# Kernel optimization log

Measured on AMD Instinct MI355X. Metric: run time of the kernel, lower is better.

## Reference

```python
import jax, jax.numpy as jnp
import numpy as np

B, N, K = 16, 2048, 16          # clouds, points per cloud, knn k
C_IN, C_OUT = 64, 64

def setup_inputs() -> dict:
    key = jax.random.key(0)
    ks = jax.random.split(key, 8)
    s_in = 1.0 / np.sqrt(C_IN)
    return {
        "x": jax.random.normal(ks[0], (B * N, C_IN), jnp.float32),
        "pos": jax.random.normal(ks[1], (B * N, 3), jnp.float32),
        "batch": jnp.repeat(jnp.arange(B, dtype=jnp.int32), N),
        "W_pos": jax.random.normal(ks[2], (3, C_OUT), jnp.float32) / np.sqrt(3.0),
        "b_pos": jnp.zeros((C_OUT,), jnp.float32),
        "W_attn": jax.random.normal(ks[3], (C_OUT, C_OUT), jnp.float32) / np.sqrt(C_OUT),
        "b_attn": jnp.zeros((C_OUT,), jnp.float32),
        "W_val": jax.random.normal(ks[4], (C_IN, C_OUT), jnp.float32) * s_in,
        "W_src": jax.random.normal(ks[5], (C_IN, C_OUT), jnp.float32) * s_in,
        "W_dst": jax.random.normal(ks[6], (C_IN, C_OUT), jnp.float32) * s_in,
    }

def _gather(a, idx):
    # a: [B, N, D], idx: [B, N, K+1] -> [B, N, K+1, D]
    return jax.vmap(lambda ab, ib: ab[ib])(a, idx)

def reference(x, pos, batch, W_pos, b_pos, W_attn, b_attn, W_val, W_src, W_dst):
    # batch is assumed contiguous with equal-size clouds (B clouds of N points),
    # so batch-restricted knn_graph == per-cloud knn after reshape.
    posr = pos.reshape(B, N, 3)
    xr = x.reshape(B, N, C_IN)
    # knn_graph(loop=False): exclude self, then PointTransformerConv re-adds self loops
    d2 = jnp.sum((posr[:, :, None, :] - posr[:, None, :, :]) ** 2, axis=-1)  # [B,N,N]
    d2 = d2 + jnp.eye(N, dtype=d2.dtype) * 1e10
    _, nbr = jax.lax.top_k(-d2, K)                                # [B,N,K] sources j per target i
    self_idx = jnp.broadcast_to(jnp.arange(N)[None, :, None], (B, N, 1))
    nbr = jnp.concatenate([nbr, self_idx], axis=2)                # self loop -> [B,N,K+1]
    alpha_i = xr @ W_dst                                          # lin_dst(x_i)  [B,N,C_OUT]
    alpha_j = _gather(xr @ W_src, nbr)                            # lin_src(x_j)  [B,N,K+1,C_OUT]
    val_j = _gather(xr @ W_val, nbr)                              # lin(x_j)
    pos_j = _gather(posr, nbr)                                    # [B,N,K+1,3]
    delta = (posr[:, :, None, :] - pos_j) @ W_pos + b_pos         # pos_nn(pos_i - pos_j)
    alpha = alpha_i[:, :, None, :] - alpha_j + delta              # subtraction attention
    alpha = alpha @ W_attn + b_attn                               # attn_nn
    alpha = jax.nn.softmax(alpha, axis=2)                         # segment softmax per target i
    out = jnp.sum(alpha * (val_j + delta), axis=2)                # weighted scatter-sum
    return out.reshape(B * N, C_OUT)
```

## Files before the change

kernel.cpp:

```cpp
#include <hip/hip_runtime.h>
#include <math.h>

#define BBATCH 16
#define NPC    2048
#define KNBR   16
#define NPTS   (BBATCH*NPC)
#define NGEMM  512
#define NKNN   512
#define BUFCAP 512

__global__ __launch_bounds__(1024) void prep_kernel(
    const float* __restrict__ Wpos, const float* __restrict__ bpos,
    const float* __restrict__ Wattn, const float* __restrict__ battn,
    const float* __restrict__ Wsrc, const float* __restrict__ Wdst,
    float* __restrict__ Hd, float* __restrict__ Hs,
    float* __restrict__ WP2, float* __restrict__ bb) {
  __shared__ float sW[4096];
  __shared__ float sD[4096];
  __shared__ float sS[4096];
  int t = threadIdx.x;
  ((float4*)sW)[t] = ((const float4*)Wattn)[t];
  ((float4*)sD)[t] = ((const float4*)Wdst)[t];
  ((float4*)sS)[t] = ((const float4*)Wsrc)[t];
  __syncthreads();
  int c = t & 63, r0 = t >> 6;
#pragma unroll
  for (int q = 0; q < 4; ++q) {
    int r = r0 + 16 * q;
    float ad = 0.f, as = 0.f;
    for (int d = 0; d < 64; ++d) {
      float w = sW[d * 64 + c];
      ad += sD[r * 64 + d] * w;
      as += sS[r * 64 + d] * w;
    }
    Hd[r * 64 + c] = ad;
    Hs[r * 64 + c] = as;
  }
  if (t < 64) {
    for (int rr = 0; rr < 3; ++rr) {
      float a = 0.f;
      for (int d = 0; d < 64; ++d) a += Wpos[rr * 64 + d] * sW[d * 64 + t];
      WP2[rr * 64 + t] = a;
    }
    float a = battn[t];
    for (int d = 0; d < 64; ++d) a += bpos[d] * sW[d * 64 + t];
    bb[t] = a;
  }
}

__global__ __launch_bounds__(1024) void gemm_kernel(
    const float* __restrict__ x, const float* __restrict__ Hd,
    const float* __restrict__ Hs, const float* __restrict__ Wval,
    float* __restrict__ A2, float* __restrict__ S2, float* __restrict__ V) {
  __shared__ __align__(16) float smem[16384];
  int t = threadIdx.x;
  int bid = blockIdx.x;
  int c = t & 63, g = t >> 6;

  float* R0 = smem;
  float* R1 = smem + 4096;
  float* R2 = smem + 8192;
  float* R3 = smem + 12288;
  ((float4*)R0)[t] = ((const float4*)(x + (size_t)bid * 64 * 64))[t];
  ((float4*)R1)[t] = ((const float4*)Hd)[t];
  ((float4*)R2)[t] = ((const float4*)Hs)[t];
  ((float4*)R3)[t] = ((const float4*)Wval)[t];
  __syncthreads();

  float v0 = 0, v1 = 0, v2 = 0, v3 = 0;
  float a0 = 0, a1 = 0, a2 = 0, a3 = 0;
  float s0 = 0, s1 = 0, s2 = 0, s3 = 0;
  const float4* xr0 = (const float4*)(R0 + (g * 4 + 0) * 64);
  const float4* xr1 = (const float4*)(R0 + (g * 4 + 1) * 64);
  const float4* xr2 = (const float4*)(R0 + (g * 4 + 2) * 64);
  const float4* xr3 = (const float4*)(R0 + (g * 4 + 3) * 64);
#pragma unroll 4
  for (int k4 = 0; k4 < 16; ++k4) {
    float4 q0 = xr0[k4], q1 = xr1[k4], q2 = xr2[k4], q3 = xr3[k4];
#pragma unroll
    for (int kk = 0; kk < 4; ++kk) {
      int k = k4 * 4 + kk;
      float wv = R3[k * 64 + c];
      float wa = R1[k * 64 + c];
      float ws = R2[k * 64 + c];
      float e0 = (kk == 0) ? q0.x : (kk == 1) ? q0.y : (kk == 2) ? q0.z : q0.w;
      float e1 = (kk == 0) ? q1.x : (kk == 1) ? q1.y : (kk == 2) ? q1.z : q1.w;
      float e2 = (kk == 0) ? q2.x : (kk == 1) ? q2.y : (kk == 2) ? q2.z : q2.w;
      float e3 = (kk == 0) ? q3.x : (kk == 1) ? q3.y : (kk == 2) ? q3.z : q3.w;
      v0 += e0 * wv; v1 += e1 * wv; v2 += e2 * wv; v3 += e3 * wv;
      a0 += e0 * wa; a1 += e1 * wa; a2 += e2 * wa; a3 += e3 * wa;
      s0 += e0 * ws; s1 += e1 * ws; s2 += e2 * ws; s3 += e3 * ws;
    }
  }
  size_t o0 = ((size_t)bid * 64 + g * 4 + 0) * 64 + c;
  V[o0] = v0; A2[o0] = a0; S2[o0] = s0;
  size_t o1 = o0 + 64;  V[o1] = v1; A2[o1] = a1; S2[o1] = s1;
  size_t o2 = o0 + 128; V[o2] = v2; A2[o2] = a2; S2[o2] = s2;
  size_t o3 = o0 + 192; V[o3] = v3; A2[o3] = a3; S2[o3] = s3;
}

__global__ __launch_bounds__(1024) void knn_edge_kernel(
    const float* __restrict__ pos, const float* __restrict__ A2,
    const float* __restrict__ S2, const float* __restrict__ V,
    const float* __restrict__ WP2, const float* __restrict__ bbv,
    const float* __restrict__ Wpos, const float* __restrict__ bpos,
    float* __restrict__ out) {
  __shared__ __align__(16) char smem[49152];
  int t = threadIdx.x;
  int kb = blockIdx.x;
  int c = t & 63, g = t >> 6;

  float4* pos4 = (float4*)smem;
  unsigned short* buf = (unsigned short*)(smem + 32768);
  int cloud = kb >> 5;
  const float* pc = pos + (size_t)cloud * NPC * 3;
  for (int p = t; p < NPC; p += 1024)
    pos4[p] = make_float4(pc[3 * p], pc[3 * p + 1], pc[3 * p + 2], 0.f);
  __syncthreads();

  int w = g, lane = c;
  for (int u = 0; u < 4; ++u) {
    int lt = u * 16 + w;
    int gi = kb * 64 + lt;
    int ti = gi & (NPC - 1);
    float4 tp = pos4[ti];
    float tx = tp.x, ty = tp.y, tz = tp.z;

    int bkt[32];
#pragma unroll
    for (int cc = 0; cc < 32; ++cc) {
      int j = cc * 64 + lane;
      float4 q = pos4[j];
      float dx = tx - q.x, dy = ty - q.y, dz = tz - q.z;
      float d2 = dx * dx + dy * dy + dz * dz;
      int b = (int)(__float_as_uint(d2) >> 20) - 896;
      bkt[cc] = max(0, min(255, b));
    }

    int lo = 0, hi = 255;
    for (int it = 0; it < 8; ++it) {
      int mid = (lo + hi) >> 1;
      int cnt = 0;
#pragma unroll
      for (int cc = 0; cc < 32; ++cc)
        cnt += (int)__popcll(__ballot(bkt[cc] <= mid));
      if (cnt >= 17) hi = mid; else lo = mid + 1;
    }
    int Tp1 = min(hi + 1, 255);

    int base = 0;
#pragma unroll
    for (int cc = 0; cc < 32; ++cc) {
      bool f = (bkt[cc] <= Tp1);
      unsigned long long mm = __ballot(f);
      unsigned int pre = __builtin_amdgcn_mbcnt_hi(
          (unsigned)(mm >> 32), __builtin_amdgcn_mbcnt_lo((unsigned)mm, 0u));
      if (f) {
        int p = base + (int)pre;
        if (p < BUFCAP) buf[w * BUFCAP + p] = (unsigned short)(cc * 64 + lane);
      }
      base += (int)__popcll(mm);
    }
    int n = min(base, BUFCAP);
    double txd = (double)tx, tyd = (double)ty, tzd = (double)tz;

    int jv;
    if (n <= 64) {
      unsigned long long gb = 0xFFFFFFFFFFFFFFFFull;
      int gj = 0x40000000 + lane;
      if (lane < n) {
        int j = buf[w * BUFCAP + lane];
        if (j != ti) {
          float4 q = pos4[j];
          double dx = __dsub_rn(txd, (double)q.x);
          double dy = __dsub_rn(tyd, (double)q.y);
          double dz = __dsub_rn(tzd, (double)q.z);
          double d2 = __dadd_rn(__dadd_rn(__dmul_rn(dx, dx), __dmul_rn(dy, dy)),
                                __dmul_rn(dz, dz));
          gb = (unsigned long long)__double_as_longlong(d2);
          gj = j;
        }
      }
      for (int k = 2; k <= 64; k <<= 1) {
        for (int jj = k >> 1; jj > 0; jj >>= 1) {
          unsigned long long ob = __shfl_xor(gb, jj);
          int oj = __shfl_xor(gj, jj);
          bool keepmin = (((lane & k) == 0) == ((lane & jj) == 0));
          bool less = (ob < gb) || (ob == gb && oj < gj);
          if (keepmin == less) { gb = ob; gj = oj; }
        }
      }
      jv = gj;
    } else {
      unsigned long long kb2[8];
      int id2[8];
#pragma unroll
      for (int r = 0; r < 8; ++r) {
        int e = r * 64 + lane;
        kb2[r] = 0xFFFFFFFFFFFFFFFFull;
        id2[r] = 0x40000000 + e;
        if (e < n) {
          int j = buf[w * BUFCAP + e];
          if (j != ti) {
            float4 q = pos4[j];
            double dx = __dsub_rn(txd, (double)q.x);
            double dy = __dsub_rn(tyd, (double)q.y);
            double dz = __dsub_rn(tzd, (double)q.z);
            double d2 = __dadd_rn(
                __dadd_rn(__dmul_rn(dx, dx), __dmul_rn(dy, dy)),
                __dmul_rn(dz, dz));
            kb2[r] = (unsigned long long)__double_as_longlong(d2);
            id2[r] = j;
          }
        }
      }
      jv = 0;
      for (int r = 0; r < KNBR; ++r) {
        unsigned long long lb = kb2[0];
        int lj = id2[0];
#pragma unroll
        for (int cc = 1; cc < 8; ++cc)
          if (kb2[cc] < lb || (kb2[cc] == lb && id2[cc] < lj)) {
            lb = kb2[cc]; lj = id2[cc];
          }
        unsigned long long gb2 = lb;
        int gj2 = lj;
#pragma unroll
        for (int d = 32; d >= 1; d >>= 1) {
          unsigned long long ob = __shfl_xor(gb2, d);
          int oj = __shfl_xor(gj2, d);
          if (ob < gb2 || (ob == gb2 && oj < gj2)) { gb2 = ob; gj2 = oj; }
        }
#pragma unroll
        for (int cc = 0; cc < 8; ++cc)
          if (id2[cc] == gj2) kb2[cc] = 0xFFFFFFFFFFFFFFFFull;
        if (lane == r) jv = gj2;
      }
    }

    {
      size_t cbase = (size_t)cloud * NPC;
      float a2v = A2[((size_t)gi) * 64 + lane];
      float wp0 = WP2[lane], wp1 = WP2[64 + lane], wp2 = WP2[128 + lane];
      float bbc = bbv[lane];
      float u0 = Wpos[lane], u1 = Wpos[64 + lane], u2 = Wpos[128 + lane];
      float bpc = bpos[lane];
      float m = -1e30f, den = 0.f, acc = 0.f;
#pragma unroll
      for (int e = 0; e < 17; ++e) {
        int j = (e < 16) ? __shfl(jv, e) : ti;
        float4 q = pos4[j];
        float dx = tx - q.x, dy = ty - q.y, dz = tz - q.z;
        size_t jrow = (cbase + j) * 64 + lane;
        float s2 = S2[jrow];
        float v = V[jrow];
        float lg = a2v - s2 + dx * wp0 + dy * wp1 + dz * wp2 + bbc;
        float vl = v + dx * u0 + dy * u1 + dz * u2 + bpc;
        float mn = fmaxf(m, lg);
        float sc = __expf(m - mn);
        float wgt = __expf(lg - mn);
        den = den * sc + wgt;
        acc = acc * sc + wgt * vl;
        m = mn;
      }
      out[((size_t)gi) * 64 + lane] = acc / den;
    }
  }
}

extern "C" void kernel_launch(void* const* d_in, const int* in_sizes, int n_in,
                              void* d_out, int out_size, void* d_ws, size_t ws_size,
                              hipStream_t stream) {
  const float* x     = (const float*)d_in[0];
  const float* pos   = (const float*)d_in[1];
  const float* Wpos  = (const float*)d_in[3];
  const float* bpos  = (const float*)d_in[4];
  const float* Wattn = (const float*)d_in[5];
  const float* battn = (const float*)d_in[6];
  const float* Wval  = (const float*)d_in[7];
  const float* Wsrc  = (const float*)d_in[8];
  const float* Wdst  = (const float*)d_in[9];

  float* ws  = (float*)d_ws;
  float* A2  = ws;
  float* S2  = A2 + (size_t)NPTS * 64;
  float* V   = S2 + (size_t)NPTS * 64;
  float* WP2 = V + (size_t)NPTS * 64;
  float* bb  = WP2 + 192;
  float* Hd  = bb + 64;
  float* Hs  = Hd + 4096;
  float* out = (float*)d_out;

  prep_kernel<<<1, 1024, 0, stream>>>(Wpos, bpos, Wattn, battn, Wsrc, Wdst,
                                      Hd, Hs, WP2, bb);
  gemm_kernel<<<NGEMM, 1024, 0, stream>>>(x, Hd, Hs, Wval, A2, S2, V);
  knn_edge_kernel<<<NKNN, 1024, 0, stream>>>(pos, A2, S2, V, WP2, bb,
                                             Wpos, bpos, out);
}
```

Measured before the change: 209.0 us.

## Fuse prep, GEMM and kNN-edge kernels into one cooperative kernel with grid sync

Turns the three kernels into device functions and calls them from a single cooperative mega-kernel. Grid-wide syncs separate the weight-prep, projection GEMM and kNN/attention phases, so only one kernel is launched instead of three. The aim is to cut the launch gaps and tail effects between stages. The fused path is used only if the occupancy query reports at least 2 resident blocks of 1024 threads per CU; otherwise it falls back to the original three launches. Grid syncs add their own cost, and the shared 64KB LDS allocation plus combined register pressure may lower occupancy.

```diff
diff --git a/kernel.cpp b/kernel.cpp
--- a/kernel.cpp
+++ b/kernel.cpp
@@ -1,5 +1,8 @@
 #include <hip/hip_runtime.h>
+#include <hip/hip_cooperative_groups.h>
 #include <math.h>
+
+namespace cg = cooperative_groups;
 
 #define BBATCH 16
 #define NPC    2048
@@ -9,16 +12,16 @@
 #define NKNN   512
 #define BUFCAP 512
 
-__global__ __launch_bounds__(1024) void prep_kernel(
+__device__ __forceinline__ void prep_body(
+    char* smem, int t,
     const float* __restrict__ Wpos, const float* __restrict__ bpos,
     const float* __restrict__ Wattn, const float* __restrict__ battn,
     const float* __restrict__ Wsrc, const float* __restrict__ Wdst,
     float* __restrict__ Hd, float* __restrict__ Hs,
     float* __restrict__ WP2, float* __restrict__ bb) {
-  __shared__ float sW[4096];
-  __shared__ float sD[4096];
-  __shared__ float sS[4096];
-  int t = threadIdx.x;
+  float* sW = (float*)smem;
+  float* sD = (float*)(smem + 16384);
+  float* sS = (float*)(smem + 32768);
   ((float4*)sW)[t] = ((const float4*)Wattn)[t];
   ((float4*)sD)[t] = ((const float4*)Wdst)[t];
   ((float4*)sS)[t] = ((const float4*)Wsrc)[t];
@@ -48,15 +51,13 @@
   }
 }
 
-__global__ __launch_bounds__(1024) void gemm_kernel(
+__device__ __forceinline__ void gemm_body(
+    char* smemc, int t, int bid,
     const float* __restrict__ x, const float* __restrict__ Hd,
     const float* __restrict__ Hs, const float* __restrict__ Wval,
     float* __restrict__ A2, float* __restrict__ S2, float* __restrict__ V) {
-  __shared__ __align__(16) float smem[16384];
-  int t = threadIdx.x;
-  int bid = blockIdx.x;
+  float* smem = (float*)smemc;
   int c = t & 63, g = t >> 6;
-
   float* R0 = smem;
   float* R1 = smem + 4096;
   float* R2 = smem + 8192;
@@ -99,17 +100,14 @@
   size_t o3 = o0 + 192; V[o3] = v3; A2[o3] = a3; S2[o3] = s3;
 }
 
-__global__ __launch_bounds__(1024) void knn_edge_kernel(
+__device__ __forceinline__ void knn_edge_body(
+    char* smem, int t, int kb,
     const float* __restrict__ pos, const float* __restrict__ A2,
     const float* __restrict__ S2, const float* __restrict__ V,
     const float* __restrict__ WP2, const float* __restrict__ bbv,
     const float* __restrict__ Wpos, const float* __restrict__ bpos,
     float* __restrict__ out) {
-  __shared__ __align__(16) char smem[49152];
-  int t = threadIdx.x;
-  int kb = blockIdx.x;
   int c = t & 63, g = t >> 6;
-
   float4* pos4 = (float4*)smem;
   unsigned short* buf = (unsigned short*)(smem + 32768);
   int cloud = kb >> 5;
@@ -268,6 +266,61 @@
   }
 }
 
+__global__ __launch_bounds__(1024) void mega_kernel(
+    const float* __restrict__ pos, const float* __restrict__ x,
+    const float* __restrict__ Wpos, const float* __restrict__ bpos,
+    const float* __restrict__ Wattn, const float* __restrict__ battn,
+    const float* __restrict__ Wval, const float* __restrict__ Wsrc,
+    const float* __restrict__ Wdst,
+    float* __restrict__ A2, float* __restrict__ S2, float* __restrict__ V,
+    float* __restrict__ WP2, float* __restrict__ bb,
+    float* __restrict__ Hd, float* __restrict__ Hs,
+    float* __restrict__ out) {
+  __shared__ __align__(16) char smem[65536];
+  cg::grid_group grid = cg::this_grid();
+  int t = threadIdx.x;
+  int bid = blockIdx.x;
+
+  if (bid == 0)
+    prep_body(smem, t, Wpos, bpos, Wattn, battn, Wsrc, Wdst, Hd, Hs, WP2, bb);
+  grid.sync();
+
+  gemm_body(smem, t, bid, x, Hd, Hs, Wval, A2, S2, V);
+  grid.sync();
+
+  knn_edge_body(smem, t, bid, pos, A2, S2, V, WP2, bb, Wpos, bpos, out);
+}
+
+__global__ __launch_bounds__(1024) void prep_kernel(
+    const float* __restrict__ Wpos, const float* __restrict__ bpos,
+    const float* __restrict__ Wattn, const float* __restrict__ battn,
+    const float* __restrict__ Wsrc, const float* __restrict__ Wdst,
+    float* __restrict__ Hd, float* __restrict__ Hs,
+    float* __restrict__ WP2, float* __restrict__ bb) {
+  __shared__ __align__(16) char smem[49152];
+  prep_body(smem, threadIdx.x, Wpos, bpos, Wattn, battn, Wsrc, Wdst,
+            Hd, Hs, WP2, bb);
+}
+
+__global__ __launch_bounds__(1024) void gemm_kernel(
+    const float* __restrict__ x, const float* __restrict__ Hd,
+    const float* __restrict__ Hs, const float* __restrict__ Wval,
+    float* __restrict__ A2, float* __restrict__ S2, float* __restrict__ V) {
+  __shared__ __align__(16) char smem[65536];
+  gemm_body(smem, threadIdx.x, blockIdx.x, x, Hd, Hs, Wval, A2, S2, V);
+}
+
+__global__ __launch_bounds__(1024) void knn_edge_kernel(
+    const float* __restrict__ pos, const float* __restrict__ A2,
+    const float* __restrict__ S2, const float* __restrict__ V,
+    const float* __restrict__ WP2, const float* __restrict__ bbv,
+    const float* __restrict__ Wpos, const float* __restrict__ bpos,
+    float* __restrict__ out) {
+  __shared__ __align__(16) char smem[49152];
+  knn_edge_body(smem, threadIdx.x, blockIdx.x, pos, A2, S2, V, WP2, bbv,
+                Wpos, bpos, out);
+}
+
 extern "C" void kernel_launch(void* const* d_in, const int* in_sizes, int n_in,
                               void* d_out, int out_size, void* d_ws, size_t ws_size,
                               hipStream_t stream) {
@@ -291,9 +344,27 @@
   float* Hs  = Hd + 4096;
   float* out = (float*)d_out;
 
-  prep_kernel<<<1, 1024, 0, stream>>>(Wpos, bpos, Wattn, battn, Wsrc, Wdst,
-                                      Hd, Hs, WP2, bb);
-  gemm_kernel<<<NGEMM, 1024, 0, stream>>>(x, Hd, Hs, Wval, A2, S2, V);
-  knn_edge_kernel<<<NKNN, 1024, 0, stream>>>(pos, A2, S2, V, WP2, bb,
-                                             Wpos, bpos, out);
-}
+  static int coop_ok = -1;
+  if (coop_ok < 0) {
+    int nb = 0;
+    hipError_t e =
+        hipOccupancyMaxActiveBlocksPerMultiprocessor(&nb, mega_kernel, 1024, 0);
+    coop_ok = (e == hipSuccess && nb >= 2) ? 1 : 0;
+  }
+
+  if (coop_ok) {
+    void* args[] = {
+        (void*)&pos, (void*)&x, (void*)&Wpos, (void*)&bpos, (void*)&Wattn,
+        (void*)&battn, (void*)&Wval, (void*)&Wsrc, (void*)&Wdst,
+        (void*)&A2, (void*)&S2, (void*)&V, (void*)&WP2, (void*)&bb,
+        (void*)&Hd, (void*)&Hs, (void*)&out};
+    hipLaunchCooperativeKernel((const void*)mega_kernel, dim3(NKNN),
+                               dim3(1024), args, 0, stream);
+  } else {
+    prep_kernel<<<1, 1024, 0, stream>>>(Wpos, bpos, Wattn, battn, Wsrc, Wdst,
+                                        Hd, Hs, WP2, bb);
+    gemm_kernel<<<NGEMM, 1024, 0, stream>>>(x, Hd, Hs, Wval, A2, S2, V);
+    knn_edge_kernel<<<NKNN, 1024, 0, stream>>>(pos, A2, S2, V, WP2, bb,
+                                               Wpos, bpos, out);
+  }
+}
```

Result: faster. 202.3 us (-3.2%).

## Fuse prep, GEMM and kNN-edge stages into one persistent kernel with per-cloud counters

Applied to the files above, without the earlier changes.

Merges the three launches into a single kernel. Each block recomputes the folded Wattn products itself, runs its GEMM tile, and signals a per-cloud atomic counter. It then does its kNN selection and spins on the counter until all 32 GEMM blocks of its cloud have finished before the edge aggregation step. This removes two launch boundaries and lets the kNN search overlap with other blocks' GEMM work. The cost is redundant weight-folding in every block, a memset per call, and a deadlock risk if the 512 blocks cannot all be resident; an occupancy check with a fallback to the old three-kernel path guards against that.

```diff
diff --git a/kernel.cpp b/kernel.cpp
--- a/kernel.cpp
+++ b/kernel.cpp
@@ -9,110 +9,110 @@
 #define NKNN   512
 #define BUFCAP 512
 
-__global__ __launch_bounds__(1024) void prep_kernel(
+__global__ __launch_bounds__(1024) void mono_kernel(
+    const float* __restrict__ pos, const float* __restrict__ x,
     const float* __restrict__ Wpos, const float* __restrict__ bpos,
     const float* __restrict__ Wattn, const float* __restrict__ battn,
-    const float* __restrict__ Wsrc, const float* __restrict__ Wdst,
-    float* __restrict__ Hd, float* __restrict__ Hs,
-    float* __restrict__ WP2, float* __restrict__ bb) {
-  __shared__ float sW[4096];
-  __shared__ float sD[4096];
-  __shared__ float sS[4096];
-  int t = threadIdx.x;
-  ((float4*)sW)[t] = ((const float4*)Wattn)[t];
-  ((float4*)sD)[t] = ((const float4*)Wdst)[t];
-  ((float4*)sS)[t] = ((const float4*)Wsrc)[t];
-  __syncthreads();
-  int c = t & 63, r0 = t >> 6;
-#pragma unroll
-  for (int q = 0; q < 4; ++q) {
-    int r = r0 + 16 * q;
-    float ad = 0.f, as = 0.f;
-    for (int d = 0; d < 64; ++d) {
-      float w = sW[d * 64 + c];
-      ad += sD[r * 64 + d] * w;
-      as += sS[r * 64 + d] * w;
-    }
-    Hd[r * 64 + c] = ad;
-    Hs[r * 64 + c] = as;
-  }
-  if (t < 64) {
-    for (int rr = 0; rr < 3; ++rr) {
-      float a = 0.f;
-      for (int d = 0; d < 64; ++d) a += Wpos[rr * 64 + d] * sW[d * 64 + t];
-      WP2[rr * 64 + t] = a;
-    }
-    float a = battn[t];
-    for (int d = 0; d < 64; ++d) a += bpos[d] * sW[d * 64 + t];
-    bb[t] = a;
-  }
-}
-
-__global__ __launch_bounds__(1024) void gemm_kernel(
-    const float* __restrict__ x, const float* __restrict__ Hd,
-    const float* __restrict__ Hs, const float* __restrict__ Wval,
-    float* __restrict__ A2, float* __restrict__ S2, float* __restrict__ V) {
-  __shared__ __align__(16) float smem[16384];
+    const float* __restrict__ Wval, const float* __restrict__ Wsrc,
+    const float* __restrict__ Wdst,
+    float* __restrict__ A2, float* __restrict__ S2, float* __restrict__ V,
+    int* __restrict__ cnt, float* __restrict__ out) {
+  __shared__ __align__(16) char smem[65536];
   int t = threadIdx.x;
   int bid = blockIdx.x;
   int c = t & 63, g = t >> 6;
-
-  float* R0 = smem;
-  float* R1 = smem + 4096;
-  float* R2 = smem + 8192;
-  float* R3 = smem + 12288;
-  ((float4*)R0)[t] = ((const float4*)(x + (size_t)bid * 64 * 64))[t];
-  ((float4*)R1)[t] = ((const float4*)Hd)[t];
-  ((float4*)R2)[t] = ((const float4*)Hs)[t];
-  ((float4*)R3)[t] = ((const float4*)Wval)[t];
-  __syncthreads();
-
-  float v0 = 0, v1 = 0, v2 = 0, v3 = 0;
-  float a0 = 0, a1 = 0, a2 = 0, a3 = 0;
-  float s0 = 0, s1 = 0, s2 = 0, s3 = 0;
-  const float4* xr0 = (const float4*)(R0 + (g * 4 + 0) * 64);
-  const float4* xr1 = (const float4*)(R0 + (g * 4 + 1) * 64);
-  const float4* xr2 = (const float4*)(R0 + (g * 4 + 2) * 64);
-  const float4* xr3 = (const float4*)(R0 + (g * 4 + 3) * 64);
+  int cloud = bid >> 5;
+
+  float* R0 = (float*)smem;
+  float* R1 = (float*)(smem + 16384);
+  float* R2 = (float*)(smem + 32768);
+  float* R3 = (float*)(smem + 49152);
+  float4* R04 = (float4*)R0;
+  float4* R34 = (float4*)R3;
+
+  R34[t] = ((const float4*)Wattn)[t];
+  R04[t] = ((const float4*)Wdst)[t];
+  __syncthreads();
+  {
+    float a0 = 0, a1 = 0, a2 = 0, a3 = 0;
+    for (int k = 0; k < 64; ++k) {
+      float w = R3[k * 64 + c];
+      a0 += R0[(g * 4 + 0) * 64 + k] * w;
+      a1 += R0[(g * 4 + 1) * 64 + k] * w;
+      a2 += R0[(g * 4 + 2) * 64 + k] * w;
+      a3 += R0[(g * 4 + 3) * 64 + k] * w;
+    }
+    R1[(g * 4 + 0) * 64 + c] = a0; R1[(g * 4 + 1) * 64 + c] = a1;
+    R1[(g * 4 + 2) * 64 + c] = a2; R1[(g * 4 + 3) * 64 + c] = a3;
+  }
+  float wpc0 = 0.f, wpc1 = 0.f, wpc2 = 0.f, bbc = battn[c];
+  for (int d = 0; d < 64; ++d) {
+    float w = R3[d * 64 + c];
+    wpc0 += Wpos[d] * w;
+    wpc1 += Wpos[64 + d] * w;
+    wpc2 += Wpos[128 + d] * w;
+    bbc += bpos[d] * w;
+  }
+  __syncthreads();
+  R04[t] = ((const float4*)Wsrc)[t];
+  __syncthreads();
+  {
+    float a0 = 0, a1 = 0, a2 = 0, a3 = 0;
+    for (int k = 0; k < 64; ++k) {
+      float w = R3[k * 64 + c];
+      a0 += R0[(g * 4 + 0) * 64 + k] * w;
+      a1 += R0[(g * 4 + 1) * 64 + k] * w;
+      a2 += R0[(g * 4 + 2) * 64 + k] * w;
+      a3 += R0[(g * 4 + 3) * 64 + k] * w;
+    }
+    R2[(g * 4 + 0) * 64 + c] = a0; R2[(g * 4 + 1) * 64 + c] = a1;
+    R2[(g * 4 + 2) * 64 + c] = a2; R2[(g * 4 + 3) * 64 + c] = a3;
+  }
+  __syncthreads();
+  R34[t] = ((const float4*)Wval)[t];
+  R04[t] = ((const float4*)(x + (size_t)bid * 64 * 64))[t];
+  __syncthreads();
+  {
+    float v0 = 0, v1 = 0, v2 = 0, v3 = 0;
+    float a0 = 0, a1 = 0, a2 = 0, a3 = 0;
+    float s0 = 0, s1 = 0, s2 = 0, s3 = 0;
+    const float4* xr0 = (const float4*)(R0 + (g * 4 + 0) * 64);
+    const float4* xr1 = (const float4*)(R0 + (g * 4 + 1) * 64);
+    const float4* xr2 = (const float4*)(R0 + (g * 4 + 2) * 64);
+    const float4* xr3 = (const float4*)(R0 + (g * 4 + 3) * 64);
 #pragma unroll 4
-  for (int k4 = 0; k4 < 16; ++k4) {
-    float4 q0 = xr0[k4], q1 = xr1[k4], q2 = xr2[k4], q3 = xr3[k4];
-#pragma unroll
-    for (int kk = 0; kk < 4; ++kk) {
-      int k = k4 * 4 + kk;
-      float wv = R3[k * 64 + c];
-      float wa = R1[k * 64 + c];
-      float ws = R2[k * 64 + c];
-      float e0 = (kk == 0) ? q0.x : (kk == 1) ? q0.y : (kk == 2) ? q0.z : q0.w;
-      float e1 = (kk == 0) ? q1.x : (kk == 1) ? q1.y : (kk == 2) ? q1.z : q1.w;
-      float e2 = (kk == 0) ? q2.x : (kk == 1) ? q2.y : (kk == 2) ? q2.z : q2.w;
-      float e3 = (kk == 0) ? q3.x : (kk == 1) ? q3.y : (kk == 2) ? q3.z : q3.w;
-      v0 += e0 * wv; v1 += e1 * wv; v2 += e2 * wv; v3 += e3 * wv;
-      a0 += e0 * wa; a1 += e1 * wa; a2 += e2 * wa; a3 += e3 * wa;
-      s0 += e0 * ws; s1 += e1 * ws; s2 += e2 * ws; s3 += e3 * ws;
-    }
-  }
-  size_t o0 = ((size_t)bid * 64 + g * 4 + 0) * 64 + c;
-  V[o0] = v0; A2[o0] = a0; S2[o0] = s0;
-  size_t o1 = o0 + 64;  V[o1] = v1; A2[o1] = a1; S2[o1] = s1;
-  size_t o2 = o0 + 128; V[o2] = v2; A2[o2] = a2; S2[o2] = s2;
-  size_t o3 = o0 + 192; V[o3] = v3; A2[o3] = a3; S2[o3] = s3;
-}
-
-__global__ __launch_bounds__(1024) void knn_edge_kernel(
-    const float* __restrict__ pos, const float* __restrict__ A2,
-    const float* __restrict__ S2, const float* __restrict__ V,
-    const float* __restrict__ WP2, const float* __restrict__ bbv,
-    const float* __restrict__ Wpos, const float* __restrict__ bpos,
-    float* __restrict__ out) {
-  __shared__ __align__(16) char smem[49152];
-  int t = threadIdx.x;
-  int kb = blockIdx.x;
-  int c = t & 63, g = t >> 6;
-
+    for (int k4 = 0; k4 < 16; ++k4) {
+      float4 q0 = xr0[k4], q1 = xr1[k4], q2 = xr2[k4], q3 = xr3[k4];
+#pragma unroll
+      for (int kk = 0; kk < 4; ++kk) {
+        int k = k4 * 4 + kk;
+        float wv = R3[k * 64 + c];
+        float wa = R1[k * 64 + c];
+        float ws = R2[k * 64 + c];
+        float e0 = (kk == 0) ? q0.x : (kk == 1) ? q0.y : (kk == 2) ? q0.z : q0.w;
+        float e1 = (kk == 0) ? q1.x : (kk == 1) ? q1.y : (kk == 2) ? q1.z : q1.w;
+        float e2 = (kk == 0) ? q2.x : (kk == 1) ? q2.y : (kk == 2) ? q2.z : q2.w;
+        float e3 = (kk == 0) ? q3.x : (kk == 1) ? q3.y : (kk == 2) ? q3.z : q3.w;
+        v0 += e0 * wv; v1 += e1 * wv; v2 += e2 * wv; v3 += e3 * wv;
+        a0 += e0 * wa; a1 += e1 * wa; a2 += e2 * wa; a3 += e3 * wa;
+        s0 += e0 * ws; s1 += e1 * ws; s2 += e2 * ws; s3 += e3 * ws;
+      }
+    }
+    size_t o0 = ((size_t)bid * 64 + g * 4 + 0) * 64 + c;
+    V[o0] = v0; A2[o0] = a0; S2[o0] = s0;
+    size_t o1 = o0 + 64;  V[o1] = v1; A2[o1] = a1; S2[o1] = s1;
+    size_t o2 = o0 + 128; V[o2] = v2; A2[o2] = a2; S2[o2] = s2;
+    size_t o3 = o0 + 192; V[o3] = v3; A2[o3] = a3; S2[o3] = s3;
+  }
+  __threadfence();
+  __syncthreads();
+  if (t == 0)
+    __hip_atomic_fetch_add(&cnt[cloud], 1, __ATOMIC_RELEASE,
+                           __HIP_MEMORY_SCOPE_AGENT);
+
+  int kb = bid;
   float4* pos4 = (float4*)smem;
   unsigned short* buf = (unsigned short*)(smem + 32768);
-  int cloud = kb >> 5;
   const float* pc = pos + (size_t)cloud * NPC * 3;
   for (int p = t; p < NPC; p += 1024)
     pos4[p] = make_float4(pc[3 * p], pc[3 * p + 1], pc[3 * p + 2], 0.f);
@@ -140,11 +140,11 @@
     int lo = 0, hi = 255;
     for (int it = 0; it < 8; ++it) {
       int mid = (lo + hi) >> 1;
-      int cnt = 0;
+      int cnt2 = 0;
 #pragma unroll
       for (int cc = 0; cc < 32; ++cc)
-        cnt += (int)__popcll(__ballot(bkt[cc] <= mid));
-      if (cnt >= 17) hi = mid; else lo = mid + 1;
+        cnt2 += (int)__popcll(__ballot(bkt[cc] <= mid));
+      if (cnt2 >= 17) hi = mid; else lo = mid + 1;
     }
     int Tp1 = min(hi + 1, 255);
 
@@ -238,6 +238,273 @@
       }
     }
 
+    if (u == 0) {
+      if (t == 0) {
+        while (__hip_atomic_load(&cnt[cloud], __ATOMIC_RELAXED,
+                                 __HIP_MEMORY_SCOPE_AGENT) < 32)
+          __builtin_amdgcn_s_sleep(8);
+        (void)__hip_atomic_load(&cnt[cloud], __ATOMIC_ACQUIRE,
+                                __HIP_MEMORY_SCOPE_AGENT);
+      }
+      __syncthreads();
+    }
+
+    {
+      size_t cbase = (size_t)cloud * NPC;
+      float a2v = A2[((size_t)gi) * 64 + lane];
+      float u0 = Wpos[lane], u1 = Wpos[64 + lane], u2 = Wpos[128 + lane];
+      float bpc = bpos[lane];
+      float m = -1e30f, den = 0.f, acc = 0.f;
+#pragma unroll
+      for (int e = 0; e < 17; ++e) {
+        int j = (e < 16) ? __shfl(jv, e) : ti;
+        float4 q = pos4[j];
+        float dx = tx - q.x, dy = ty - q.y, dz = tz - q.z;
+        size_t jrow = (cbase + j) * 64 + lane;
+        float s2 = S2[jrow];
+        float v = V[jrow];
+        float lg = a2v - s2 + dx * wpc0 + dy * wpc1 + dz * wpc2 + bbc;
+        float vl = v + dx * u0 + dy * u1 + dz * u2 + bpc;
+        float mn = fmaxf(m, lg);
+        float sc = __expf(m - mn);
+        float wgt = __expf(lg - mn);
+        den = den * sc + wgt;
+        acc = acc * sc + wgt * vl;
+        m = mn;
+      }
+      out[((size_t)gi) * 64 + lane] = acc / den;
+    }
+  }
+}
+
+__global__ __launch_bounds__(1024) void prep_kernel(
+    const float* __restrict__ Wpos, const float* __restrict__ bpos,
+    const float* __restrict__ Wattn, const float* __restrict__ battn,
+    const float* __restrict__ Wsrc, const float* __restrict__ Wdst,
+    float* __restrict__ Hd, float* __restrict__ Hs,
+    float* __restrict__ WP2, float* __restrict__ bb) {
+  __shared__ float sW[4096];
+  __shared__ float sD[4096];
+  __shared__ float sS[4096];
+  int t = threadIdx.x;
+  ((float4*)sW)[t] = ((const float4*)Wattn)[t];
+  ((float4*)sD)[t] = ((const float4*)Wdst)[t];
+  ((float4*)sS)[t] = ((const float4*)Wsrc)[t];
+  __syncthreads();
+  int c = t & 63, r0 = t >> 6;
+#pragma unroll
+  for (int q = 0; q < 4; ++q) {
+    int r = r0 + 16 * q;
+    float ad = 0.f, as = 0.f;
+    for (int d = 0; d < 64; ++d) {
+      float w = sW[d * 64 + c];
+      ad += sD[r * 64 + d] * w;
+      as += sS[r * 64 + d] * w;
+    }
+    Hd[r * 64 + c] = ad;
+    Hs[r * 64 + c] = as;
+  }
+  if (t < 64) {
+    for (int rr = 0; rr < 3; ++rr) {
+      float a = 0.f;
+      for (int d = 0; d < 64; ++d) a += Wpos[rr * 64 + d] * sW[d * 64 + t];
+      WP2[rr * 64 + t] = a;
+    }
+    float a = battn[t];
+    for (int d = 0; d < 64; ++d) a += bpos[d] * sW[d * 64 + t];
+    bb[t] = a;
+  }
+}
+
+__global__ __launch_bounds__(1024) void gemm_kernel(
+    const float* __restrict__ x, const float* __restrict__ Hd,
+    const float* __restrict__ Hs, const float* __restrict__ Wval,
+    float* __restrict__ A2, float* __restrict__ S2, float* __restrict__ V) {
+  __shared__ __align__(16) float smem[16384];
+  int t = threadIdx.x;
+  int bid = blockIdx.x;
+  int c = t & 63, g = t >> 6;
+  float* R0 = smem;
+  float* R1 = smem + 4096;
+  float* R2 = smem + 8192;
+  float* R3 = smem + 12288;
+  ((float4*)R0)[t] = ((const float4*)(x + (size_t)bid * 64 * 64))[t];
+  ((float4*)R1)[t] = ((const float4*)Hd)[t];
+  ((float4*)R2)[t] = ((const float4*)Hs)[t];
+  ((float4*)R3)[t] = ((const float4*)Wval)[t];
+  __syncthreads();
+
+  float v0 = 0, v1 = 0, v2 = 0, v3 = 0;
+  float a0 = 0, a1 = 0, a2 = 0, a3 = 0;
+  float s0 = 0, s1 = 0, s2 = 0, s3 = 0;
+  const float4* xr0 = (const float4*)(R0 + (g * 4 + 0) * 64);
+  const float4* xr1 = (const float4*)(R0 + (g * 4 + 1) * 64);
+  const float4* xr2 = (const float4*)(R0 + (g * 4 + 2) * 64);
+  const float4* xr3 = (const float4*)(R0 + (g * 4 + 3) * 64);
+#pragma unroll 4
+  for (int k4 = 0; k4 < 16; ++k4) {
+    float4 q0 = xr0[k4], q1 = xr1[k4], q2 = xr2[k4], q3 = xr3[k4];
+#pragma unroll
+    for (int kk = 0; kk < 4; ++kk) {
+      int k = k4 * 4 + kk;
+      float wv = R3[k * 64 + c];
+      float wa = R1[k * 64 + c];
+      float ws = R2[k * 64 + c];
+      float e0 = (kk == 0) ? q0.x : (kk == 1) ? q0.y : (kk == 2) ? q0.z : q0.w;
+      float e1 = (kk == 0) ? q1.x : (kk == 1) ? q1.y : (kk == 2) ? q1.z : q1.w;
+      float e2 = (kk == 0) ? q2.x : (kk == 1) ? q2.y : (kk == 2) ? q2.z : q2.w;
+      float e3 = (kk == 0) ? q3.x : (kk == 1) ? q3.y : (kk == 2) ? q3.z : q3.w;
+      v0 += e0 * wv; v1 += e1 * wv; v2 += e2 * wv; v3 += e3 * wv;
+      a0 += e0 * wa; a1 += e1 * wa; a2 += e2 * wa; a3 += e3 * wa;
+      s0 += e0 * ws; s1 += e1 * ws; s2 += e2 * ws; s3 += e3 * ws;
+    }
+  }
+  size_t o0 = ((size_t)bid * 64 + g * 4 + 0) * 64 + c;
+  V[o0] = v0; A2[o0] = a0; S2[o0] = s0;
+  size_t o1 = o0 + 64;  V[o1] = v1; A2[o1] = a1; S2[o1] = s1;
+  size_t o2 = o0 + 128; V[o2] = v2; A2[o2] = a2; S2[o2] = s2;
+  size_t o3 = o0 + 192; V[o3] = v3; A2[o3] = a3; S2[o3] = s3;
+}
+
+__global__ __launch_bounds__(1024) void knn_edge_kernel(
+    const float* __restrict__ pos, const float* __restrict__ A2,
+    const float* __restrict__ S2, const float* __restrict__ V,
+    const float* __restrict__ WP2, const float* __restrict__ bbv,
+    const float* __restrict__ Wpos, const float* __restrict__ bpos,
+    float* __restrict__ out) {
+  __shared__ __align__(16) char smem[49152];
+  int t = threadIdx.x;
+  int kb = blockIdx.x;
+  int c = t & 63, g = t >> 6;
+
+  float4* pos4 = (float4*)smem;
+  unsigned short* buf = (unsigned short*)(smem + 32768);
+  int cloud = kb >> 5;
+  const float* pc = pos + (size_t)cloud * NPC * 3;
+  for (int p = t; p < NPC; p += 1024)
+    pos4[p] = make_float4(pc[3 * p], pc[3 * p + 1], pc[3 * p + 2], 0.f);
+  __syncthreads();
+
+  int w = g, lane = c;
+  for (int u = 0; u < 4; ++u) {
+    int lt = u * 16 + w;
+    int gi = kb * 64 + lt;
+    int ti = gi & (NPC - 1);
+    float4 tp = pos4[ti];
+    float tx = tp.x, ty = tp.y, tz = tp.z;
+
+    int bkt[32];
+#pragma unroll
+    for (int cc = 0; cc < 32; ++cc) {
+      int j = cc * 64 + lane;
+      float4 q = pos4[j];
+      float dx = tx - q.x, dy = ty - q.y, dz = tz - q.z;
+      float d2 = dx * dx + dy * dy + dz * dz;
+      int b = (int)(__float_as_uint(d2) >> 20) - 896;
+      bkt[cc] = max(0, min(255, b));
+    }
+
+    int lo = 0, hi = 255;
+    for (int it = 0; it < 8; ++it) {
+      int mid = (lo + hi) >> 1;
+      int cnt = 0;
+#pragma unroll
+      for (int cc = 0; cc < 32; ++cc)
+        cnt += (int)__popcll(__ballot(bkt[cc] <= mid));
+      if (cnt >= 17) hi = mid; else lo = mid + 1;
+    }
+    int Tp1 = min(hi + 1, 255);
+
+    int base = 0;
+#pragma unroll
+    for (int cc = 0; cc < 32; ++cc) {
+      bool f = (bkt[cc] <= Tp1);
+      unsigned long long mm = __ballot(f);
+      unsigned int pre = __builtin_amdgcn_mbcnt_hi(
+          (unsigned)(mm >> 32), __builtin_amdgcn_mbcnt_lo((unsigned)mm, 0u));
+      if (f) {
+        int p = base + (int)pre;
+        if (p < BUFCAP) buf[w * BUFCAP + p] = (unsigned short)(cc * 64 + lane);
+      }
+      base += (int)__popcll(mm);
+    }
+    int n = min(base, BUFCAP);
+    double txd = (double)tx, tyd = (double)ty, tzd = (double)tz;
+
+    int jv;
+    if (n <= 64) {
+      unsigned long long gb = 0xFFFFFFFFFFFFFFFFull;
+      int gj = 0x40000000 + lane;
+      if (lane < n) {
+        int j = buf[w * BUFCAP + lane];
+        if (j != ti) {
+          float4 q = pos4[j];
+          double dx = __dsub_rn(txd, (double)q.x);
+          double dy = __dsub_rn(tyd, (double)q.y);
+          double dz = __dsub_rn(tzd, (double)q.z);
+          double d2 = __dadd_rn(__dadd_rn(__dmul_rn(dx, dx), __dmul_rn(dy, dy)),
+                                __dmul_rn(dz, dz));
+          gb = (unsigned long long)__double_as_longlong(d2);
+          gj = j;
+        }
+      }
+      for (int k = 2; k <= 64; k <<= 1) {
+        for (int jj = k >> 1; jj > 0; jj >>= 1) {
+          unsigned long long ob = __shfl_xor(gb, jj);
+          int oj = __shfl_xor(gj, jj);
+          bool keepmin = (((lane & k) == 0) == ((lane & jj) == 0));
+          bool less = (ob < gb) || (ob == gb && oj < gj);
+          if (keepmin == less) { gb = ob; gj = oj; }
+        }
+      }
+      jv = gj;
+    } else {
+      unsigned long long kb2[8];
+      int id2[8];
+#pragma unroll
+      for (int r = 0; r < 8; ++r) {
+        int e = r * 64 + lane;
+        kb2[r] = 0xFFFFFFFFFFFFFFFFull;
+        id2[r] = 0x40000000 + e;
+        if (e < n) {
+          int j = buf[w * BUFCAP + e];
+          if (j != ti) {
+            float4 q = pos4[j];
+            double dx = __dsub_rn(txd, (double)q.x);
+            double dy = __dsub_rn(tyd, (double)q.y);
+            double dz = __dsub_rn(tzd, (double)q.z);
+            double d2 = __dadd_rn(
+                __dadd_rn(__dmul_rn(dx, dx), __dmul_rn(dy, dy)),
+                __dmul_rn(dz, dz));
+            kb2[r] = (unsigned long long)__double_as_longlong(d2);
+            id2[r] = j;
+          }
+        }
+      }
+      jv = 0;
+      for (int r = 0; r < KNBR; ++r) {
+        unsigned long long lb = kb2[0];
+        int lj = id2[0];
+#pragma unroll
+        for (int cc = 1; cc < 8; ++cc)
+          if (kb2[cc] < lb || (kb2[cc] == lb && id2[cc] < lj)) {
+            lb = kb2[cc]; lj = id2[cc];
+          }
+        unsigned long long gb2 = lb;
+        int gj2 = lj;
+#pragma unroll
+        for (int d = 32; d >= 1; d >>= 1) {
+          unsigned long long ob = __shfl_xor(gb2, d);
+          int oj = __shfl_xor(gj2, d);
+          if (ob < gb2 || (ob == gb2 && oj < gj2)) { gb2 = ob; gj2 = oj; }
+        }
+#pragma unroll
+        for (int cc = 0; cc < 8; ++cc)
+          if (id2[cc] == gj2) kb2[cc] = 0xFFFFFFFFFFFFFFFFull;
+        if (lane == r) jv = gj2;
+      }
+    }
+
     {
       size_t cbase = (size_t)cloud * NPC;
       float a2v = A2[((size_t)gi) * 64 + lane];
@@ -289,11 +556,27 @@
   float* bb  = WP2 + 192;
   float* Hd  = bb + 64;
   float* Hs  = Hd + 4096;
+  int*   cnt = (int*)(Hs + 4096);
   float* out = (float*)d_out;
 
-  prep_kernel<<<1, 1024, 0, stream>>>(Wpos, bpos, Wattn, battn, Wsrc, Wdst,
-                                      Hd, Hs, WP2, bb);
-  gemm_kernel<<<NGEMM, 1024, 0, stream>>>(x, Hd, Hs, Wval, A2, S2, V);
-  knn_edge_kernel<<<NKNN, 1024, 0, stream>>>(pos, A2, S2, V, WP2, bb,
-                                             Wpos, bpos, out);
+  static int mono_ok = -1;
+  if (mono_ok < 0) {
+    int nb = 0;
+    hipError_t e =
+        hipOccupancyMaxActiveBlocksPerMultiprocessor(&nb, mono_kernel, 1024, 0);
+    mono_ok = (e == hipSuccess && nb >= 2) ? 1 : 0;
+  }
+
+  if (mono_ok) {
+    hipMemsetAsync(cnt, 0, 16 * sizeof(int), stream);
+    mono_kernel<<<NKNN, 1024, 0, stream>>>(pos, x, Wpos, bpos, Wattn, battn,
+                                           Wval, Wsrc, Wdst, A2, S2, V, cnt,
+                                           out);
+  } else {
+    prep_kernel<<<1, 1024, 0, stream>>>(Wpos, bpos, Wattn, battn, Wsrc, Wdst,
+                                        Hd, Hs, WP2, bb);
+    gemm_kernel<<<NGEMM, 1024, 0, stream>>>(x, Hd, Hs, Wval, A2, S2, V);
+    knn_edge_kernel<<<NKNN, 1024, 0, stream>>>(pos, A2, S2, V, WP2, bb,
+                                               Wpos, bpos, out);
+  }
 }
```

Result: no change. 209.0 us (+0.0%).
